# Performance work log

Hardware: AMD Instinct MI355X
Metric: run time of the kernel (lower is better)

Reference implementation:

```python
import jax, jax.numpy as jnp
import numpy as np

B, NPER, K, H = 256, 512, 8, 16  # events, particles/event, knn k, hidden_dim
N = B * NPER


def _edge_conv(h, Wc, bc):
    """DynamicEdgeConv: per-event kNN graph, edge MLP on [x_i, x_j-x_i], max-aggregate."""
    d = h.shape[-1]
    hb = h.reshape(B, NPER, d)
    sq = jnp.sum(hb * hb, axis=-1)                                   # [B,n]
    d2 = sq[:, :, None] + sq[:, None, :] - 2.0 * jnp.einsum('bnd,bmd->bnm', hb, hb)
    _, idx = jax.lax.top_k(-d2, K)                                   # [B,n,K] nearest (incl. self)
    xj = jax.vmap(lambda hh, ii: hh[ii])(hb, idx)                    # [B,n,K,d] gather
    xi = jnp.broadcast_to(hb[:, :, None, :], xj.shape)               # [B,n,K,d]
    e = jnp.concatenate([xi, xj - xi], axis=-1)                      # [B,n,K,2d]
    m = jax.nn.elu(e @ Wc + bc)                                      # [B,n,K,H]
    return jnp.max(m, axis=2).reshape(N, -1)                         # scatter-max over neighbors


def setup_inputs() -> dict:
    key = jax.random.key(0)
    ks = jax.random.split(key, 10)
    def lin(k, fin, fout):
        return jax.random.normal(k, (fin, fout), jnp.float32) / np.sqrt(fin)
    x_pf = jax.random.normal(ks[0], (N, 4), jnp.float32)
    batch_pf = jnp.repeat(jnp.arange(B, dtype=jnp.int64), NPER)
    return {
        'x_pf': x_pf, 'batch_pf': batch_pf,
        'W1': lin(ks[1], 4, H),  'b1': jnp.zeros((H,), jnp.float32),
        'W2': lin(ks[2], H, H),  'b2': jnp.zeros((H,), jnp.float32),
        'Wc': lin(ks[3], 2 * H, H), 'bc': jnp.zeros((H,), jnp.float32),
        'Wo1': lin(ks[4], H, 8), 'bo1': jnp.zeros((8,), jnp.float32),
        'Wo2': lin(ks[5], 8, 4), 'bo2': jnp.zeros((4,), jnp.float32),
        'Wo3': lin(ks[6], 4, 1), 'bo3': jnp.zeros((1,), jnp.float32),
    }


def reference(x_pf, batch_pf, W1, b1, W2, b2, Wc, bc, Wo1, bo1, Wo2, bo2, Wo3, bo3):
    # pf_encode: Linear-ELU-Linear-ELU (assumes contiguous equal-size events per batch_pf)
    h = jax.nn.elu(x_pf @ W1 + b1)
    h = jax.nn.elu(h @ W2 + b2)                                      # [N,H]
    # two DynamicEdgeConv passes with SHARED weights (same self.conv called twice)
    f1 = _edge_conv(h, Wc, bc)
    f2 = _edge_conv(f1, Wc, bc)
    # avg_pool_x with cluster == batch -> per-event mean
    pooled = f2.reshape(B, NPER, -1).mean(axis=1)                    # [B,H]
    o = jax.nn.elu(pooled @ Wo1 + bo1)
    o = jax.nn.elu(o @ Wo2 + bo2)
    out = o @ Wo3 + bo3                                              # [B,1]
    return out, jnp.arange(B)
```

## Files before the change

kernel.cpp:

```cpp
#include <hip/hip_runtime.h>

#define NEV 256
#define NP  512
#define HD  16
#define KBS 36

typedef short s16x8  __attribute__((ext_vector_type(8)));
typedef float f32x16 __attribute__((ext_vector_type(16)));

#define Z16 {0.f,0.f,0.f,0.f,0.f,0.f,0.f,0.f,0.f,0.f,0.f,0.f,0.f,0.f,0.f,0.f}

__device__ __forceinline__ float elu_f(float x) {
    return x > 0.0f ? x : (__expf(x) - 1.0f);
}
__device__ __forceinline__ unsigned umin_(unsigned a, unsigned b) { return a < b ? a : b; }
__device__ __forceinline__ unsigned med3u(unsigned a, unsigned b, unsigned c) {
    unsigned d;
    asm("v_med3_u32 %0, %1, %2, %3" : "=v"(d) : "v"(a), "v"(b), "v"(c));
    return d;
}
__device__ __forceinline__ unsigned short rneb(float f) {
    unsigned u = __float_as_uint(f);
    return (unsigned short)((u + 0x7FFFu + ((u >> 16) & 1u)) >> 16);
}
__device__ __forceinline__ float bits2f(unsigned short b) {
    return __uint_as_float(((unsigned)b) << 16);
}
__device__ __forceinline__ unsigned sx32(unsigned v) {
    return (unsigned)__shfl_xor((int)v, 32, 64);
}

__global__ __launch_bounds__(1024, 4) void suep_fused(
    const float* __restrict__ x_pf,
    const float* __restrict__ W1,  const float* __restrict__ b1,
    const float* __restrict__ W2,  const float* __restrict__ b2,
    const float* __restrict__ Wc,  const float* __restrict__ bc,
    const float* __restrict__ Wo1, const float* __restrict__ bo1,
    const float* __restrict__ Wo2, const float* __restrict__ bo2,
    const float* __restrict__ Wo3, const float* __restrict__ bo3,
    float* __restrict__ out)
{
    __shared__ unsigned kb[NP * KBS];
    __shared__ s16x8 fragH[16][64];
    __shared__ s16x8 fragL[16][64];
    __shared__ float sSq[NP];
    __shared__ float sW1[64], sB1[HD], sW2[256], sB2[HD];
    __shared__ float sWcB[256], sWcD[256], sBc[HD];
    __shared__ float sWo1[128], sBo1[8], sWo2[32], sBo2[4], sWo3[4], sBo3[1];
    __shared__ float sRedM[8];
    __shared__ float sRed[16][HD];
    __shared__ float sPool[HD];

    const int tid = threadIdx.x, ev = blockIdx.x;
    const int l = tid & 63, w = tid >> 6;
    const int n = tid & 511;
    const bool loT = (tid < 512);
    const int c32 = l & 31, kh = l >> 5;
    const int row = 32 * w + c32;

    if (tid < 64) sW1[tid] = W1[tid];
    if (tid < HD) { sB1[tid] = b1[tid]; sB2[tid] = b2[tid]; sBc[tid] = bc[tid]; }
    if (tid < 256) {
        sW2[tid] = W2[tid];
        float wb = Wc[256 + tid];
        sWcB[tid] = wb;
        sWcD[tid] = Wc[tid] - wb;
    }
    if (tid < 128) sWo1[tid] = Wo1[tid];
    if (tid < 8)   sBo1[tid] = bo1[tid];
    if (tid < 32)  sWo2[tid] = Wo2[tid];
    if (tid < 4)   { sBo2[tid] = bo2[tid]; sWo3[tid] = Wo3[tid]; }
    if (tid == 0)  sBo3[0] = bo3[0];
    __syncthreads();

    float hr[HD];
    {
        float4 xv = ((const float4*)x_pf)[ev * NP + n];
        float e1[HD];
#pragma unroll
        for (int c = 0; c < HD; ++c) {
            float a = sB1[c];
            a = fmaf(xv.x, sW1[0 * HD + c], a);
            a = fmaf(xv.y, sW1[1 * HD + c], a);
            a = fmaf(xv.z, sW1[2 * HD + c], a);
            a = fmaf(xv.w, sW1[3 * HD + c], a);
            e1[c] = elu_f(a);
        }
#pragma unroll
        for (int c = 0; c < HD; ++c) {
            float a = sB2[c];
#pragma unroll
            for (int f = 0; f < HD; ++f) a = fmaf(e1[f], sW2[f * HD + c], a);
            hr[c] = elu_f(a);
        }
    }

    auto build_frags = [&]() -> float {
        s16x8 v0, v1;
        float sq = 0.0f;
#pragma unroll
        for (int k = 0; k < HD; ++k) {
            unsigned short hb = rneb(hr[k]);
            float fh = bits2f(hb);
            unsigned short lb = rneb(hr[k] - fh);
            if (loT) {
                float ht = fh + bits2f(lb);
                sq = fmaf(ht, ht, sq);
            }
            unsigned short vb = loT ? hb : lb;
            if (k < 8) v0[k] = (short)vb; else v1[k - 8] = (short)vb;
        }
        s16x8 (*fr)[64] = loT ? fragH : fragL;
        fr[n >> 5][n & 31]      = v0;
        fr[n >> 5][(n & 31) + 32] = v1;
        if (loT) {
            sSq[n] = sq;
            float m = sq;
#pragma unroll
            for (int d = 32; d >= 1; d >>= 1) m = fmaxf(m, __shfl_xor(m, d, 64));
            if (l == 0) sRedM[w] = m;
        }
        __syncthreads();
        float mx = sRedM[0];
#pragma unroll
        for (int i = 1; i < 8; ++i) mx = fmaxf(mx, sRedM[i]);
        return mx + 1.0f;
    };

    auto do_conv = [&](bool last) {
        float Cv = build_frags();

        s16x8 Ah = fragH[w][l], Al = fragL[w][l];

        unsigned t0 = ~0u, t1 = ~0u, t2 = ~0u, t3 = ~0u,
                 t4 = ~0u, t5 = ~0u, t6 = ~0u, t7 = ~0u;
#define INS(KEY) do { unsigned kk = (KEY);              \
        t7 = med3u(t6, kk, t7); t6 = med3u(t5, kk, t6); \
        t5 = med3u(t4, kk, t5); t4 = med3u(t3, kk, t4); \
        t3 = med3u(t2, kk, t3); t2 = med3u(t1, kk, t2); \
        t1 = med3u(t0, kk, t1); t0 = umin_(kk, t0); } while (0)

        auto cs = [&](int s, f32x16& a) {
            s16x8 Bh = fragH[s][l], Bl = fragL[s][l];
            f32x16 z = Z16;
            a = __builtin_amdgcn_mfma_f32_32x32x16_bf16(Al, Bh, z, 0, 0, 0);
            a = __builtin_amdgcn_mfma_f32_32x32x16_bf16(Ah, Bl, a, 0, 0, 0);
            a = __builtin_amdgcn_mfma_f32_32x32x16_bf16(Ah, Bh, a, 0, 0, 0);
        };

        unsigned* wp = &kb[(32 * w + 4 * kh) * KBS + c32];
        auto st = [&](int s, const f32x16& a) {
            float base = Cv + sSq[32 * s + c32];
            unsigned colb = (unsigned)(32 * s + c32);
#pragma unroll
            for (int q = 0; q < 16; ++q) {
                const int roff = (q & 3) + 8 * (q >> 2);
                wp[roff * KBS] =
                    (__float_as_uint(fmaf(-2.0f, a[q], base)) & 0xFFFFFE00u) | colb;
            }
        };

        const uint4* rp = (const uint4*)&kb[row * KBS + 16 * kh];
        auto scan = [&]() {
#pragma unroll
            for (int g = 0; g < 4; ++g) {
                uint4 k4 = rp[g];
                INS(k4.x); INS(k4.y); INS(k4.z); INS(k4.w);
            }
        };

        f32x16 a0, a1;
        cs(0, a0);
        for (int s = 0; s < 16; s += 2) {
            st(s, a0);
            cs(s + 1, a1);
            asm volatile("s_waitcnt lgkmcnt(0)" ::: "memory");
            scan();
            st(s + 1, a1);
            if (s + 2 < 16) cs(s + 2, a0);
            asm volatile("s_waitcnt lgkmcnt(0)" ::: "memory");
            scan();
        }
#undef INS

        unsigned m0 = umin_(t0, sx32(t7)), m1 = umin_(t1, sx32(t6)),
                 m2 = umin_(t2, sx32(t5)), m3 = umin_(t3, sx32(t4)),
                 m4 = umin_(t4, sx32(t3)), m5 = umin_(t5, sx32(t2)),
                 m6 = umin_(t6, sx32(t1)), m7 = umin_(t7, sx32(t0));

        float gb[HD];
        {
            const float* Wm = loT ? sWcB : sWcD;
#pragma unroll
            for (int c = 0; c < HD; ++c) gb[c] = loT ? 0.0f : sBc[c];
#pragma unroll
            for (int f = 0; f < HD; ++f) {
                float hf = hr[f];
#pragma unroll
                for (int c = 0; c < HD; ++c) gb[c] = fmaf(hf, Wm[f * HD + c], gb[c]);
            }
        }
        __syncthreads();
        float* gr = (float*)&kb[n * KBS + (loT ? 0 : 16)];
        ((float4*)gr)[0] = make_float4(gb[0], gb[1], gb[2], gb[3]);
        ((float4*)gr)[1] = make_float4(gb[4], gb[5], gb[6], gb[7]);
        ((float4*)gr)[2] = make_float4(gb[8], gb[9], gb[10], gb[11]);
        ((float4*)gr)[3] = make_float4(gb[12], gb[13], gb[14], gb[15]);
        __syncthreads();

        int j0 = (int)((kh ? m4 : m0) & 511u), j1 = (int)((kh ? m5 : m1) & 511u);
        int j2 = (int)((kh ? m6 : m2) & 511u), j3 = (int)((kh ? m7 : m3) & 511u);
        float z[HD];
        {
            const float4* g0 = (const float4*)&kb[j0 * KBS];
            const float4* g1 = (const float4*)&kb[j1 * KBS];
            const float4* g2 = (const float4*)&kb[j2 * KBS];
            const float4* g3 = (const float4*)&kb[j3 * KBS];
#pragma unroll
            for (int qq = 0; qq < 4; ++qq) {
                float4 va = g0[qq], vb = g1[qq], vc = g2[qq], vd = g3[qq];
                z[4*qq+0] = fmaxf(fmaxf(va.x, vb.x), fmaxf(vc.x, vd.x));
                z[4*qq+1] = fmaxf(fmaxf(va.y, vb.y), fmaxf(vc.y, vd.y));
                z[4*qq+2] = fmaxf(fmaxf(va.z, vb.z), fmaxf(vc.z, vd.z));
                z[4*qq+3] = fmaxf(fmaxf(va.w, vb.w), fmaxf(vc.w, vd.w));
            }
        }
#pragma unroll
        for (int c = 0; c < HD; ++c) z[c] = fmaxf(z[c], __shfl_xor(z[c], 32, 64));

        float fo[HD];
        if (kh == 0) {
            const float4* br = (const float4*)&kb[row * KBS + 16];
#pragma unroll
            for (int qq = 0; qq < 4; ++qq) {
                float4 vb = br[qq];
                fo[4*qq+0] = elu_f(z[4*qq+0] + vb.x);
                fo[4*qq+1] = elu_f(z[4*qq+1] + vb.y);
                fo[4*qq+2] = elu_f(z[4*qq+2] + vb.z);
                fo[4*qq+3] = elu_f(z[4*qq+3] + vb.w);
            }
        }

        if (!last) {
            __syncthreads();
            if (kh == 0) {
                float4* fr = (float4*)&kb[row * KBS];
                fr[0] = make_float4(fo[0], fo[1], fo[2], fo[3]);
                fr[1] = make_float4(fo[4], fo[5], fo[6], fo[7]);
                fr[2] = make_float4(fo[8], fo[9], fo[10], fo[11]);
                fr[3] = make_float4(fo[12], fo[13], fo[14], fo[15]);
            }
            __syncthreads();
            const float4* hrp = (const float4*)&kb[n * KBS];
#pragma unroll
            for (int qq = 0; qq < 4; ++qq) {
                float4 v = hrp[qq];
                hr[4*qq+0] = v.x; hr[4*qq+1] = v.y; hr[4*qq+2] = v.z; hr[4*qq+3] = v.w;
            }
        } else {
#pragma unroll
            for (int m = 16; m >= 1; m >>= 1) {
#pragma unroll
                for (int c = 0; c < HD; ++c) fo[c] += __shfl_xor(fo[c], m, 64);
            }
            if (l == 0) {
                ((float4*)(&sRed[w][0]))[0] = make_float4(fo[0], fo[1], fo[2], fo[3]);
                ((float4*)(&sRed[w][0]))[1] = make_float4(fo[4], fo[5], fo[6], fo[7]);
                ((float4*)(&sRed[w][0]))[2] = make_float4(fo[8], fo[9], fo[10], fo[11]);
                ((float4*)(&sRed[w][0]))[3] = make_float4(fo[12], fo[13], fo[14], fo[15]);
            }
            __syncthreads();
            if (tid < HD) {
                float s = 0.0f;
#pragma unroll
                for (int ww = 0; ww < 16; ++ww) s += sRed[ww][tid];
                sPool[tid] = s * (1.0f / (float)NP);
            }
            __syncthreads();
        }
    };

    do_conv(false);
    do_conv(true);

    if (tid == 0) {
        float o1[8];
#pragma unroll
        for (int c = 0; c < 8; ++c) {
            float a = sBo1[c];
#pragma unroll
            for (int f = 0; f < HD; ++f) a = fmaf(sPool[f], sWo1[f * 8 + c], a);
            o1[c] = elu_f(a);
        }
        float o2[4];
#pragma unroll
        for (int c = 0; c < 4; ++c) {
            float a = sBo2[c];
#pragma unroll
            for (int f = 0; f < 8; ++f) a = fmaf(o1[f], sWo2[f * 4 + c], a);
            o2[c] = elu_f(a);
        }
        float o3 = sBo3[0];
#pragma unroll
        for (int f = 0; f < 4; ++f) o3 = fmaf(o2[f], sWo3[f], o3);
        out[ev] = o3;
        out[NEV + ev] = (float)ev;
    }
}

extern "C" void kernel_launch(void* const* d_in, const int* in_sizes, int n_in,
                              void* d_out, int out_size, void* d_ws, size_t ws_size,
                              hipStream_t stream) {
    const float* x_pf = (const float*)d_in[0];
    const float* W1  = (const float*)d_in[2];
    const float* b1  = (const float*)d_in[3];
    const float* W2  = (const float*)d_in[4];
    const float* b2  = (const float*)d_in[5];
    const float* Wc  = (const float*)d_in[6];
    const float* bc  = (const float*)d_in[7];
    const float* Wo1 = (const float*)d_in[8];
    const float* bo1 = (const float*)d_in[9];
    const float* Wo2 = (const float*)d_in[10];
    const float* bo2 = (const float*)d_in[11];
    const float* Wo3 = (const float*)d_in[12];
    const float* bo3 = (const float*)d_in[13];
    float* out = (float*)d_out;

    hipLaunchKernelGGL(suep_fused, dim3(NEV), dim3(1024), 0, stream,
                       x_pf, W1, b1, W2, b2, Wc, bc,
                       Wo1, bo1, Wo2, bo2, Wo3, bo3, out);
}
```

Measured before the change: 145.8 us.

## Pair particle halves per wave, swizzle key buffer, keep features in registers

Each particle row is now handled by two lanes (kh halves) in the same wave, where before it was split across the lower and upper 512 threads. Both lanes compute the hi/lo bf16 split, and each scans half of the candidate columns. This removes the LDS round-trip and two barriers between the convolutions, because the output features stay in registers. The kNN key buffer gets a wider stride with XOR swizzling for the writes and the 8-byte reads, meant to cut LDS bank conflicts. The scan loop is re-pipelined so the MFMA of the next tile overlaps the scan of the previous one. Shared memory is packed into one aliased byte array, which adds the risk of overlapping regions.

```diff
diff --git a/kernel.cpp b/kernel.cpp
--- a/kernel.cpp
+++ b/kernel.cpp
@@ -3,7 +3,30 @@
 #define NEV 256
 #define NP  512
 #define HD  16
-#define KBS 36
+#define KBW 40
+#define GBW 36
+
+#define KB_OFF 0
+#define FH_OFF 81920
+#define FL_OFF 98304
+#define SQ_OFF 114688
+#define RM_OFF 116736
+#define W_OFF  116800
+#define SMEM_BYTES 121040
+
+#define O_W1 0
+#define O_B1 64
+#define O_W2 80
+#define O_B2 336
+#define O_WCB 352
+#define O_WCD 608
+#define O_BC 864
+#define O_WO1 880
+#define O_BO1 1008
+#define O_WO2 1016
+#define O_BO2 1048
+#define O_WO3 1052
+#define O_BO3 1056
 
 typedef short s16x8  __attribute__((ext_vector_type(8)));
 typedef float f32x16 __attribute__((ext_vector_type(16)));
@@ -40,182 +63,188 @@
     const float* __restrict__ Wo3, const float* __restrict__ bo3,
     float* __restrict__ out)
 {
-    __shared__ unsigned kb[NP * KBS];
-    __shared__ s16x8 fragH[16][64];
-    __shared__ s16x8 fragL[16][64];
-    __shared__ float sSq[NP];
-    __shared__ float sW1[64], sB1[HD], sW2[256], sB2[HD];
-    __shared__ float sWcB[256], sWcD[256], sBc[HD];
-    __shared__ float sWo1[128], sBo1[8], sWo2[32], sBo2[4], sWo3[4], sBo3[1];
-    __shared__ float sRedM[8];
-    __shared__ float sRed[16][HD];
-    __shared__ float sPool[HD];
+    __shared__ __align__(16) unsigned char smem[SMEM_BYTES];
+
+    unsigned* kb       = (unsigned*)(smem + KB_OFF);
+    s16x8 (*fragH)[64] = (s16x8(*)[64])(smem + FH_OFF);
+    s16x8 (*fragL)[64] = (s16x8(*)[64])(smem + FL_OFF);
+    float* gbase       = (float*)(smem + KB_OFF);
+    float* sSq         = (float*)(smem + SQ_OFF);
+    float* sRedM       = (float*)(smem + RM_OFF);
+    float* sW          = (float*)(smem + W_OFF);
+    float (*sRed)[HD]  = (float(*)[HD])(smem + W_OFF);
+    float* sPool       = sW + 256;
 
     const int tid = threadIdx.x, ev = blockIdx.x;
-    const int l = tid & 63, w = tid >> 6;
-    const int n = tid & 511;
-    const bool loT = (tid < 512);
-    const int c32 = l & 31, kh = l >> 5;
-    const int row = 32 * w + c32;
-
-    if (tid < 64) sW1[tid] = W1[tid];
-    if (tid < HD) { sB1[tid] = b1[tid]; sB2[tid] = b2[tid]; sBc[tid] = bc[tid]; }
+    const int l  = tid & 63;
+    const int w  = tid >> 6;
+    const int rl = l & 31;
+    const int kh = l >> 5;
+    const int r  = 32 * w + rl;
+
+    if (tid < 64)  sW[O_W1 + tid] = W1[tid];
+    if (tid < HD)  { sW[O_B1+tid] = b1[tid]; sW[O_B2+tid] = b2[tid]; sW[O_BC+tid] = bc[tid]; }
     if (tid < 256) {
-        sW2[tid] = W2[tid];
+        sW[O_W2 + tid] = W2[tid];
         float wb = Wc[256 + tid];
-        sWcB[tid] = wb;
-        sWcD[tid] = Wc[tid] - wb;
+        sW[O_WCB + tid] = wb;
+        sW[O_WCD + tid] = Wc[tid] - wb;
     }
-    if (tid < 128) sWo1[tid] = Wo1[tid];
-    if (tid < 8)   sBo1[tid] = bo1[tid];
-    if (tid < 32)  sWo2[tid] = Wo2[tid];
-    if (tid < 4)   { sBo2[tid] = bo2[tid]; sWo3[tid] = Wo3[tid]; }
-    if (tid == 0)  sBo3[0] = bo3[0];
+    if (tid < 128) sW[O_WO1 + tid] = Wo1[tid];
+    if (tid < 8)   sW[O_BO1 + tid] = bo1[tid];
+    if (tid < 32)  sW[O_WO2 + tid] = Wo2[tid];
+    if (tid < 4)   { sW[O_BO2+tid] = bo2[tid]; sW[O_WO3+tid] = Wo3[tid]; }
+    if (tid == 0)  sW[O_BO3] = bo3[0];
     __syncthreads();
 
     float hr[HD];
     {
-        float4 xv = ((const float4*)x_pf)[ev * NP + n];
+        float4 xv = ((const float4*)x_pf)[ev * NP + r];
         float e1[HD];
 #pragma unroll
         for (int c = 0; c < HD; ++c) {
-            float a = sB1[c];
-            a = fmaf(xv.x, sW1[0 * HD + c], a);
-            a = fmaf(xv.y, sW1[1 * HD + c], a);
-            a = fmaf(xv.z, sW1[2 * HD + c], a);
-            a = fmaf(xv.w, sW1[3 * HD + c], a);
+            float a = sW[O_B1 + c];
+            a = fmaf(xv.x, sW[O_W1 + 0*HD + c], a);
+            a = fmaf(xv.y, sW[O_W1 + 1*HD + c], a);
+            a = fmaf(xv.z, sW[O_W1 + 2*HD + c], a);
+            a = fmaf(xv.w, sW[O_W1 + 3*HD + c], a);
             e1[c] = elu_f(a);
         }
 #pragma unroll
         for (int c = 0; c < HD; ++c) {
-            float a = sB2[c];
-#pragma unroll
-            for (int f = 0; f < HD; ++f) a = fmaf(e1[f], sW2[f * HD + c], a);
+            float a = sW[O_B2 + c];
+#pragma unroll
+            for (int f = 0; f < HD; ++f) a = fmaf(e1[f], sW[O_W2 + f*HD + c], a);
             hr[c] = elu_f(a);
         }
     }
 
-    auto build_frags = [&]() -> float {
-        s16x8 v0, v1;
-        float sq = 0.0f;
-#pragma unroll
-        for (int k = 0; k < HD; ++k) {
-            unsigned short hb = rneb(hr[k]);
-            float fh = bits2f(hb);
-            unsigned short lb = rneb(hr[k] - fh);
-            if (loT) {
+    const int rho = (rl >> 3) & 3;
+    const uint2* rp0 = (const uint2*)&kb[r*KBW + (((16*kh +  0) ^ rho) & ~1)];
+    const uint2* rp1 = (const uint2*)&kb[r*KBW + (((16*kh +  2) ^ rho) & ~1)];
+    const uint2* rp2 = (const uint2*)&kb[r*KBW + (((16*kh +  4) ^ rho) & ~1)];
+    const uint2* rp3 = (const uint2*)&kb[r*KBW + (((16*kh +  6) ^ rho) & ~1)];
+    const uint2* rp4 = (const uint2*)&kb[r*KBW + (((16*kh +  8) ^ rho) & ~1)];
+    const uint2* rp5 = (const uint2*)&kb[r*KBW + (((16*kh + 10) ^ rho) & ~1)];
+    const uint2* rp6 = (const uint2*)&kb[r*KBW + (((16*kh + 12) ^ rho) & ~1)];
+    const uint2* rp7 = (const uint2*)&kb[r*KBW + (((16*kh + 14) ^ rho) & ~1)];
+    unsigned* wg0 = &kb[(32*w + 4*kh +  0)*KBW + (rl ^ 0)];
+    unsigned* wg1 = &kb[(32*w + 4*kh +  8)*KBW + (rl ^ 1)];
+    unsigned* wg2 = &kb[(32*w + 4*kh + 16)*KBW + (rl ^ 2)];
+    unsigned* wg3 = &kb[(32*w + 4*kh + 24)*KBW + (rl ^ 3)];
+
+    auto do_conv = [&](bool last) {
+        __syncthreads();
+
+        {
+            s16x8 v0, v1;
+            float sq = 0.0f;
+#pragma unroll
+            for (int k = 0; k < HD; ++k) {
+                unsigned short hb = rneb(hr[k]);
+                float fh = bits2f(hb);
+                unsigned short lb = rneb(hr[k] - fh);
                 float ht = fh + bits2f(lb);
                 sq = fmaf(ht, ht, sq);
-            }
-            unsigned short vb = loT ? hb : lb;
-            if (k < 8) v0[k] = (short)vb; else v1[k - 8] = (short)vb;
-        }
-        s16x8 (*fr)[64] = loT ? fragH : fragL;
-        fr[n >> 5][n & 31]      = v0;
-        fr[n >> 5][(n & 31) + 32] = v1;
-        if (loT) {
-            sSq[n] = sq;
+                unsigned short vb = kh ? lb : hb;
+                if (k < 8) v0[k] = (short)vb; else v1[k-8] = (short)vb;
+            }
+            s16x8 (*fr)[64] = kh ? fragL : fragH;
+            fr[w][rl]      = v0;
+            fr[w][rl + 32] = v1;
+            if (kh == 0) sSq[r] = sq;
             float m = sq;
 #pragma unroll
             for (int d = 32; d >= 1; d >>= 1) m = fmaxf(m, __shfl_xor(m, d, 64));
             if (l == 0) sRedM[w] = m;
         }
         __syncthreads();
-        float mx = sRedM[0];
-#pragma unroll
-        for (int i = 1; i < 8; ++i) mx = fmaxf(mx, sRedM[i]);
-        return mx + 1.0f;
-    };
-
-    auto do_conv = [&](bool last) {
-        float Cv = build_frags();
+        float Cv = sRedM[0];
+#pragma unroll
+        for (int i = 1; i < 16; ++i) Cv = fmaxf(Cv, sRedM[i]);
+        Cv += 1.0f;
 
         s16x8 Ah = fragH[w][l], Al = fragL[w][l];
 
-        unsigned t0 = ~0u, t1 = ~0u, t2 = ~0u, t3 = ~0u,
-                 t4 = ~0u, t5 = ~0u, t6 = ~0u, t7 = ~0u;
+        auto mm3 = [&](int s) -> f32x16 {
+            s16x8 Bh = fragH[s][l], Bl = fragL[s][l];
+            f32x16 z = Z16;
+            f32x16 a = __builtin_amdgcn_mfma_f32_32x32x16_bf16(Al, Bh, z, 0,0,0);
+            a = __builtin_amdgcn_mfma_f32_32x32x16_bf16(Ah, Bl, a, 0,0,0);
+            a = __builtin_amdgcn_mfma_f32_32x32x16_bf16(Ah, Bh, a, 0,0,0);
+            return a;
+        };
+        auto st = [&](int s, const f32x16& a) {
+            float    base = Cv + sSq[32*s + rl];
+            unsigned colb = (unsigned)(32*s + rl);
+#pragma unroll
+            for (int q = 0; q < 16; ++q) {
+                unsigned kk = (__float_as_uint(fmaf(-2.0f, a[q], base)) & 0xFFFFFE00u) | colb;
+                unsigned* wq = (q>>2)==0 ? wg0 : (q>>2)==1 ? wg1 : (q>>2)==2 ? wg2 : wg3;
+                wq[(q & 3) * KBW] = kk;
+            }
+        };
+
+        unsigned t0=~0u,t1=~0u,t2=~0u,t3=~0u,t4=~0u,t5=~0u,t6=~0u,t7=~0u;
 #define INS(KEY) do { unsigned kk = (KEY);              \
         t7 = med3u(t6, kk, t7); t6 = med3u(t5, kk, t6); \
         t5 = med3u(t4, kk, t5); t4 = med3u(t3, kk, t4); \
         t3 = med3u(t2, kk, t3); t2 = med3u(t1, kk, t2); \
         t1 = med3u(t0, kk, t1); t0 = umin_(kk, t0); } while (0)
-
-        auto cs = [&](int s, f32x16& a) {
-            s16x8 Bh = fragH[s][l], Bl = fragL[s][l];
-            f32x16 z = Z16;
-            a = __builtin_amdgcn_mfma_f32_32x32x16_bf16(Al, Bh, z, 0, 0, 0);
-            a = __builtin_amdgcn_mfma_f32_32x32x16_bf16(Ah, Bl, a, 0, 0, 0);
-            a = __builtin_amdgcn_mfma_f32_32x32x16_bf16(Ah, Bh, a, 0, 0, 0);
-        };
-
-        unsigned* wp = &kb[(32 * w + 4 * kh) * KBS + c32];
-        auto st = [&](int s, const f32x16& a) {
-            float base = Cv + sSq[32 * s + c32];
-            unsigned colb = (unsigned)(32 * s + c32);
-#pragma unroll
-            for (int q = 0; q < 16; ++q) {
-                const int roff = (q & 3) + 8 * (q >> 2);
-                wp[roff * KBS] =
-                    (__float_as_uint(fmaf(-2.0f, a[q], base)) & 0xFFFFFE00u) | colb;
-            }
-        };
-
-        const uint4* rp = (const uint4*)&kb[row * KBS + 16 * kh];
-        auto scan = [&]() {
-#pragma unroll
-            for (int g = 0; g < 4; ++g) {
-                uint4 k4 = rp[g];
-                INS(k4.x); INS(k4.y); INS(k4.z); INS(k4.w);
-            }
-        };
-
-        f32x16 a0, a1;
-        cs(0, a0);
+#define SCAN16 do { uint2 c0=rp0[0], c1=rp1[0], c2=rp2[0], c3=rp3[0], \
+                          c4=rp4[0], c5=rp5[0], c6=rp6[0], c7=rp7[0]; \
+        INS(c0.x); INS(c0.y); INS(c1.x); INS(c1.y);                   \
+        INS(c2.x); INS(c2.y); INS(c3.x); INS(c3.y);                   \
+        INS(c4.x); INS(c4.y); INS(c5.x); INS(c5.y);                   \
+        INS(c6.x); INS(c6.y); INS(c7.x); INS(c7.y); } while (0)
+
+        f32x16 accA = mm3(0), accB;
+#pragma unroll 1
         for (int s = 0; s < 16; s += 2) {
-            st(s, a0);
-            cs(s + 1, a1);
-            asm volatile("s_waitcnt lgkmcnt(0)" ::: "memory");
-            scan();
-            st(s + 1, a1);
-            if (s + 2 < 16) cs(s + 2, a0);
-            asm volatile("s_waitcnt lgkmcnt(0)" ::: "memory");
-            scan();
-        }
+            accB = mm3(s + 1);
+            if (s > 0) SCAN16;
+            st(s, accA);
+            if (s + 2 < 16) accA = mm3(s + 2);
+            SCAN16;
+            st(s + 1, accB);
+        }
+        SCAN16;
+#undef SCAN16
 #undef INS
 
         unsigned m0 = umin_(t0, sx32(t7)), m1 = umin_(t1, sx32(t6)),
-                 m2 = umin_(t2, sx32(t5)), m3 = umin_(t3, sx32(t4)),
-                 m4 = umin_(t4, sx32(t3)), m5 = umin_(t5, sx32(t2)),
-                 m6 = umin_(t6, sx32(t1)), m7 = umin_(t7, sx32(t0));
+                 m2 = umin_(t2, sx32(t5)), m3 = umin_(t3, sx32(t4));
 
         float gb[HD];
         {
-            const float* Wm = loT ? sWcB : sWcD;
-#pragma unroll
-            for (int c = 0; c < HD; ++c) gb[c] = loT ? 0.0f : sBc[c];
+            const float* Wm = kh ? (sW + O_WCD) : (sW + O_WCB);
+#pragma unroll
+            for (int c = 0; c < HD; ++c) gb[c] = kh ? sW[O_BC + c] : 0.0f;
 #pragma unroll
             for (int f = 0; f < HD; ++f) {
                 float hf = hr[f];
 #pragma unroll
-                for (int c = 0; c < HD; ++c) gb[c] = fmaf(hf, Wm[f * HD + c], gb[c]);
+                for (int c = 0; c < HD; ++c) gb[c] = fmaf(hf, Wm[f*HD + c], gb[c]);
             }
         }
         __syncthreads();
-        float* gr = (float*)&kb[n * KBS + (loT ? 0 : 16)];
-        ((float4*)gr)[0] = make_float4(gb[0], gb[1], gb[2], gb[3]);
-        ((float4*)gr)[1] = make_float4(gb[4], gb[5], gb[6], gb[7]);
-        ((float4*)gr)[2] = make_float4(gb[8], gb[9], gb[10], gb[11]);
-        ((float4*)gr)[3] = make_float4(gb[12], gb[13], gb[14], gb[15]);
+        {
+            float4* gr = (float4*)(gbase + r*GBW + 16*kh);
+            gr[0] = make_float4(gb[0],  gb[1],  gb[2],  gb[3]);
+            gr[1] = make_float4(gb[4],  gb[5],  gb[6],  gb[7]);
+            gr[2] = make_float4(gb[8],  gb[9],  gb[10], gb[11]);
+            gr[3] = make_float4(gb[12], gb[13], gb[14], gb[15]);
+        }
         __syncthreads();
 
-        int j0 = (int)((kh ? m4 : m0) & 511u), j1 = (int)((kh ? m5 : m1) & 511u);
-        int j2 = (int)((kh ? m6 : m2) & 511u), j3 = (int)((kh ? m7 : m3) & 511u);
+        int j0 = (int)(m0 & 511u), j1 = (int)(m1 & 511u);
+        int j2 = (int)(m2 & 511u), j3 = (int)(m3 & 511u);
         float z[HD];
         {
-            const float4* g0 = (const float4*)&kb[j0 * KBS];
-            const float4* g1 = (const float4*)&kb[j1 * KBS];
-            const float4* g2 = (const float4*)&kb[j2 * KBS];
-            const float4* g3 = (const float4*)&kb[j3 * KBS];
+            const float4* g0 = (const float4*)(gbase + j0*GBW);
+            const float4* g1 = (const float4*)(gbase + j1*GBW);
+            const float4* g2 = (const float4*)(gbase + j2*GBW);
+            const float4* g3 = (const float4*)(gbase + j3*GBW);
 #pragma unroll
             for (int qq = 0; qq < 4; ++qq) {
                 float4 va = g0[qq], vb = g1[qq], vc = g2[qq], vd = g3[qq];
@@ -229,8 +258,8 @@
         for (int c = 0; c < HD; ++c) z[c] = fmaxf(z[c], __shfl_xor(z[c], 32, 64));
 
         float fo[HD];
-        if (kh == 0) {
-            const float4* br = (const float4*)&kb[row * KBS + 16];
+        {
+            const float4* br = (const float4*)(gbase + r*GBW + 16);
 #pragma unroll
             for (int qq = 0; qq < 4; ++qq) {
                 float4 vb = br[qq];
@@ -242,31 +271,18 @@
         }
 
         if (!last) {
-            __syncthreads();
-            if (kh == 0) {
-                float4* fr = (float4*)&kb[row * KBS];
-                fr[0] = make_float4(fo[0], fo[1], fo[2], fo[3]);
-                fr[1] = make_float4(fo[4], fo[5], fo[6], fo[7]);
-                fr[2] = make_float4(fo[8], fo[9], fo[10], fo[11]);
-                fr[3] = make_float4(fo[12], fo[13], fo[14], fo[15]);
-            }
-            __syncthreads();
-            const float4* hrp = (const float4*)&kb[n * KBS];
-#pragma unroll
-            for (int qq = 0; qq < 4; ++qq) {
-                float4 v = hrp[qq];
-                hr[4*qq+0] = v.x; hr[4*qq+1] = v.y; hr[4*qq+2] = v.z; hr[4*qq+3] = v.w;
-            }
+#pragma unroll
+            for (int c = 0; c < HD; ++c) hr[c] = fo[c];
         } else {
 #pragma unroll
-            for (int m = 16; m >= 1; m >>= 1) {
-#pragma unroll
-                for (int c = 0; c < HD; ++c) fo[c] += __shfl_xor(fo[c], m, 64);
+            for (int d = 32; d >= 1; d >>= 1) {
+#pragma unroll
+                for (int c = 0; c < HD; ++c) fo[c] += __shfl_xor(fo[c], d, 64);
             }
             if (l == 0) {
-                ((float4*)(&sRed[w][0]))[0] = make_float4(fo[0], fo[1], fo[2], fo[3]);
-                ((float4*)(&sRed[w][0]))[1] = make_float4(fo[4], fo[5], fo[6], fo[7]);
-                ((float4*)(&sRed[w][0]))[2] = make_float4(fo[8], fo[9], fo[10], fo[11]);
+                ((float4*)(&sRed[w][0]))[0] = make_float4(fo[0],  fo[1],  fo[2],  fo[3]);
+                ((float4*)(&sRed[w][0]))[1] = make_float4(fo[4],  fo[5],  fo[6],  fo[7]);
+                ((float4*)(&sRed[w][0]))[2] = make_float4(fo[8],  fo[9],  fo[10], fo[11]);
                 ((float4*)(&sRed[w][0]))[3] = make_float4(fo[12], fo[13], fo[14], fo[15]);
             }
             __syncthreads();
@@ -274,7 +290,7 @@
                 float s = 0.0f;
 #pragma unroll
                 for (int ww = 0; ww < 16; ++ww) s += sRed[ww][tid];
-                sPool[tid] = s * (1.0f / (float)NP);
+                sPool[tid] = s * (1.0f / 1024.0f);
             }
             __syncthreads();
         }
@@ -287,22 +303,22 @@
         float o1[8];
 #pragma unroll
         for (int c = 0; c < 8; ++c) {
-            float a = sBo1[c];
-#pragma unroll
-            for (int f = 0; f < HD; ++f) a = fmaf(sPool[f], sWo1[f * 8 + c], a);
+            float a = sW[O_BO1 + c];
+#pragma unroll
+            for (int f = 0; f < HD; ++f) a = fmaf(sPool[f], sW[O_WO1 + f*8 + c], a);
             o1[c] = elu_f(a);
         }
         float o2[4];
 #pragma unroll
         for (int c = 0; c < 4; ++c) {
-            float a = sBo2[c];
-#pragma unroll
-            for (int f = 0; f < 8; ++f) a = fmaf(o1[f], sWo2[f * 4 + c], a);
+            float a = sW[O_BO2 + c];
+#pragma unroll
+            for (int f = 0; f < 8; ++f) a = fmaf(o1[f], sW[O_WO2 + f*4 + c], a);
             o2[c] = elu_f(a);
         }
-        float o3 = sBo3[0];
-#pragma unroll
-        for (int f = 0; f < 4; ++f) o3 = fmaf(o2[f], sWo3[f], o3);
+        float o3 = sW[O_BO3];
+#pragma unroll
+        for (int f = 0; f < 4; ++f) o3 = fmaf(o2[f], sW[O_WO3 + f], o3);
         out[ev] = o3;
         out[NEV + ev] = (float)ev;
     }
```

Measured after the change: 148.2 us. No clear change (+1.6%).
